# Kernel optimization log

Measured on AMD Instinct MI355X. Metric: run time of the kernel, lower is better.

Reference implementation:

```python
import jax, jax.numpy as jnp
import numpy as np
from jax import lax

BATCH, CH, SEQ, D_MODEL = 4, 8, 1024, 512
D_STATE, D_CONV, EXPAND = 16, 4, 2
D_INNER = EXPAND * D_MODEL
DT_RANK = (D_MODEL + 15) // 16  # math.ceil(d_model / 16) as in mamba_ssm


def _silu(v):
    return v * jax.nn.sigmoid(v)


def setup_inputs() -> dict:
    key = jax.random.key(0)
    ks = jax.random.split(key, 8)
    s = lambda fan: 1.0 / np.sqrt(fan)
    x = jax.random.normal(ks[0], (BATCH, CH, SEQ, D_MODEL), jnp.float32)
    W_in = jax.random.normal(ks[1], (2 * D_INNER, D_MODEL), jnp.float32) * s(D_MODEL)
    conv_w = jax.random.normal(ks[2], (D_INNER, D_CONV), jnp.float32) * s(D_CONV)
    conv_b = jnp.zeros((D_INNER,), jnp.float32)
    W_xproj = jax.random.normal(ks[3], (DT_RANK + 2 * D_STATE, D_INNER), jnp.float32) * s(D_INNER)
    W_dt = jax.random.normal(ks[4], (D_INNER, DT_RANK), jnp.float32) * s(DT_RANK)
    # dt bias ~ inverse-softplus of dt in [1e-3, 0.1] (mamba init)
    dt0 = jnp.exp(jax.random.uniform(ks[5], (D_INNER,), jnp.float32) * (np.log(0.1) - np.log(1e-3)) + np.log(1e-3))
    b_dt = dt0 + jnp.log(-jnp.expm1(-dt0))
    A_log = jnp.log(jnp.broadcast_to(jnp.arange(1, D_STATE + 1, dtype=jnp.float32), (D_INNER, D_STATE)))
    D = jnp.ones((D_INNER,), jnp.float32)
    W_out = jax.random.normal(ks[6], (D_MODEL, D_INNER), jnp.float32) * s(D_INNER)
    return {"x": x, "W_in": W_in, "conv_w": conv_w, "conv_b": conv_b,
            "W_xproj": W_xproj, "W_dt": W_dt, "b_dt": b_dt,
            "A_log": A_log, "D": D, "W_out": W_out}


def _mamba(u, W_in, conv_w, conv_b, W_xproj, W_dt, b_dt, A_log, D, W_out):
    # u: (B, L, d_model)
    Bn, L, _ = u.shape
    xz = u @ W_in.T                                  # (B, L, 2*d_inner)
    xs, z = jnp.split(xz, 2, axis=-1)
    # depthwise causal conv1d, padding=d_conv-1, truncated to L
    xt = jnp.pad(xs.transpose(0, 2, 1), ((0, 0), (0, 0), (D_CONV - 1, 0)))  # (B, d_inner, L+pad)
    xc = lax.conv_general_dilated(xt, conv_w[:, None, :], (1,), 'VALID',
                                  feature_group_count=D_INNER,
                                  dimension_numbers=('NCH', 'OIH', 'NCH'))   # (B, d_inner, L)
    xs = _silu((xc + conv_b[None, :, None]).transpose(0, 2, 1))              # (B, L, d_inner)
    x_dbl = xs @ W_xproj.T                           # (B, L, dt_rank + 2*d_state)
    dt_in = x_dbl[..., :DT_RANK]
    Bm = x_dbl[..., DT_RANK:DT_RANK + D_STATE]       # (B, L, d_state)
    Cm = x_dbl[..., DT_RANK + D_STATE:]              # (B, L, d_state)
    dt = jax.nn.softplus(dt_in @ W_dt.T + b_dt)      # (B, L, d_inner)
    A = -jnp.exp(A_log)                              # (d_inner, d_state)

    def step(h, inp):
        dt_t, B_t, C_t, x_t = inp                    # (B,di), (B,ds), (B,ds), (B,di)
        dA = jnp.exp(dt_t[..., None] * A)            # (B, di, ds)
        h = dA * h + (dt_t * x_t)[..., None] * B_t[:, None, :]
        y = jnp.einsum('bds,bs->bd', h, C_t)
        return h, y

    h0 = jnp.zeros((Bn, D_INNER, D_STATE), xs.dtype)
    xsL = (dt.transpose(1, 0, 2), Bm.transpose(1, 0, 2), Cm.transpose(1, 0, 2), xs.transpose(1, 0, 2))
    _, ys = lax.scan(step, h0, xsL)                  # ys: (L, B, d_inner)
    y = ys.transpose(1, 0, 2) + xs * D
    y = y * _silu(z)
    return y @ W_out.T                               # (B, L, d_model)


def reference(x, W_in, conv_w, conv_b, W_xproj, W_dt, b_dt, A_log, D, W_out):
    b, c, L, dm = x.shape
    # shared Mamba weights over channels -> fold channel into batch (== per-channel loop)
    u = x.reshape(b * c, L, dm)
    out = _mamba(u, W_in, conv_w, conv_b, W_xproj, W_dt, b_dt, A_log, D, W_out)
    return out.reshape(b, c, L, dm)
```

## Files before the change

kernel.cpp:

```cpp
#include <hip/hip_runtime.h>
#include <hip/hip_bf16.h>
#include <math.h>

#define BATCHN   4
#define CHN      8
#define SEQ      1024
#define DMODEL   512
#define DSTATE   16
#define DCONV    4
#define DINNER   1024
#define DTRANK   32
#define NROWS    32768
#define XD       64
#define NBC      32

#define GCH   16
#define CLEN  (SEQ / GCH)
#define SUB   32
#define PSLOT 17

#define CSPL  8
#define CTS   (SEQ / CSPL)

enum { EPI_NONE = 0, EPI_GATE = 1, EPI_GATE_PACK = 2 };

__device__ __forceinline__ float siluf(float v) {
    return v / (1.0f + expf(-v));
}
__device__ __forceinline__ float softplus_fast(float v) {
    return (v > 20.0f) ? v : __logf(1.0f + __expf(v));
}

typedef short short8 __attribute__((ext_vector_type(8)));
typedef float floatx4 __attribute__((ext_vector_type(4)));

__device__ __forceinline__ unsigned short f2bf_rne(float f) {
    unsigned int u = __float_as_uint(f);
    u += 0x7fffu + ((u >> 16) & 1u);
    return (unsigned short)(u >> 16);
}
__device__ __forceinline__ float bf2f(unsigned short h) {
    return __uint_as_float(((unsigned int)h) << 16);
}

__device__ __forceinline__ unsigned short* lds_pt(unsigned short (*arr)[32],
                                                  int row, int slot) {
    return &arr[row][(slot ^ ((row >> 1) & 3)) << 3];
}
__device__ __forceinline__ const unsigned short* lds_pt(
        const unsigned short (*arr)[32], int row, int slot) {
    return &arr[row][(slot ^ ((row >> 1) & 3)) << 3];
}

__global__ __launch_bounds__(256)
void split_w(const float* __restrict__ W, unsigned char* __restrict__ W2,
             int R, int K) {
    const int KB = K >> 5;
    const int idx = blockIdx.x * 256 + threadIdx.x;
    if (idx >= R * KB) return;
    const int row = idx / KB;
    const int kb  = idx - row * KB;
    const float* src = W + (size_t)row * K + kb * 32;
    unsigned short h[32], l[32];
#pragma unroll
    for (int e = 0; e < 32; e += 4) {
        const float4 v = *(const float4*)(src + e);
        const float vv[4] = {v.x, v.y, v.z, v.w};
#pragma unroll
        for (int q = 0; q < 4; ++q) {
            const unsigned short hi = f2bf_rne(vv[q]);
            h[e + q] = hi;
            l[e + q] = f2bf_rne(vv[q] - bf2f(hi));
        }
    }
    unsigned char* dst = W2 + ((size_t)row * KB + kb) * 128;
    union { short8 v; unsigned short u[8]; } pk;
#pragma unroll
    for (int c = 0; c < 4; ++c) {
#pragma unroll
        for (int e = 0; e < 8; ++e) pk.u[e] = h[c * 8 + e];
        *(short8*)(dst + c * 16) = pk.v;
    }
#pragma unroll
    for (int c = 0; c < 4; ++c) {
#pragma unroll
        for (int e = 0; e < 8; ++e) pk.u[e] = l[c * 8 + e];
        *(short8*)(dst + 64 + c * 16) = pk.v;
    }
}

template <bool A_PRE, bool B_PRE, int EPI>
__global__ __launch_bounds__(256, 2)
void gemm_split(const float* __restrict__ Af, const unsigned char* __restrict__ A2,
                int lda,
                const float* __restrict__ Bf, const unsigned char* __restrict__ B2,
                int ldb,
                float* __restrict__ C, int ldc,
                int K) {
    __shared__ __align__(16) unsigned short Ah[128][32];
    __shared__ __align__(16) unsigned short Al[128][32];
    __shared__ __align__(16) unsigned short Bh[128][32];
    __shared__ __align__(16) unsigned short Bl[128][32];

    const int tid  = threadIdx.x;
    const int lane = tid & 63;
    const int wv   = tid >> 6;
    const int quad = lane >> 4;
    const int m16  = lane & 15;
    const int wm   = (wv & 1) * 64;
    const int wn   = (wv >> 1) * 64;
    const int m0   = blockIdx.y * 128;
    const int n0   = blockIdx.x * 128;

    const int srow = tid >> 1;
    const int skb  = (tid & 1) * 16;
    const int ssl  = skb >> 3;

    const unsigned char* aptr = nullptr;
    const unsigned char* bptr = nullptr;
    if constexpr (A_PRE)
        aptr = A2 + (size_t)(m0 + srow) * (K >> 5) * 128 + 2 * skb;
    if constexpr (B_PRE)
        bptr = B2 + (size_t)(n0 + srow) * (K >> 5) * 128 + 2 * skb;

    floatx4 acc[4][4];
#pragma unroll
    for (int i = 0; i < 4; ++i)
#pragma unroll
        for (int j = 0; j < 4; ++j) acc[i][j] = (floatx4){0.f, 0.f, 0.f, 0.f};

    union U { short8 v; unsigned short u[8]; };

    for (int k0 = 0; k0 < K; k0 += 32) {
        short8 pa0, pa1, pa2, pa3;
        U ah0, ah1, al0, al1;
        if constexpr (A_PRE) {
            pa0 = *(const short8*)(aptr);
            pa1 = *(const short8*)(aptr + 16);
            pa2 = *(const short8*)(aptr + 64);
            pa3 = *(const short8*)(aptr + 80);
            aptr += 128;
        } else {
            const float* ap = Af + (size_t)(m0 + srow) * lda + k0 + skb;
            const float4 a0 = *(const float4*)(ap + 0);
            const float4 a1 = *(const float4*)(ap + 4);
            const float4 a2 = *(const float4*)(ap + 8);
            const float4 a3 = *(const float4*)(ap + 12);
            const float af[16] = {a0.x, a0.y, a0.z, a0.w, a1.x, a1.y, a1.z, a1.w,
                                  a2.x, a2.y, a2.z, a2.w, a3.x, a3.y, a3.z, a3.w};
#pragma unroll
            for (int e = 0; e < 8; ++e) {
                const unsigned short ha = f2bf_rne(af[e]);
                ah0.u[e] = ha; al0.u[e] = f2bf_rne(af[e] - bf2f(ha));
                const unsigned short hb = f2bf_rne(af[8 + e]);
                ah1.u[e] = hb; al1.u[e] = f2bf_rne(af[8 + e] - bf2f(hb));
            }
        }

        short8 pb0, pb1, pb2, pb3;
        U bh0, bh1, bl0, bl1;
        if constexpr (B_PRE) {
            pb0 = *(const short8*)(bptr);
            pb1 = *(const short8*)(bptr + 16);
            pb2 = *(const short8*)(bptr + 64);
            pb3 = *(const short8*)(bptr + 80);
            bptr += 128;
        } else {
            const float* bp = Bf + (size_t)(n0 + srow) * ldb + k0 + skb;
            const float4 b0 = *(const float4*)(bp + 0);
            const float4 b1 = *(const float4*)(bp + 4);
            const float4 b2 = *(const float4*)(bp + 8);
            const float4 b3 = *(const float4*)(bp + 12);
            const float bf[16] = {b0.x, b0.y, b0.z, b0.w, b1.x, b1.y, b1.z, b1.w,
                                  b2.x, b2.y, b2.z, b2.w, b3.x, b3.y, b3.z, b3.w};
#pragma unroll
            for (int e = 0; e < 8; ++e) {
                const unsigned short ha = f2bf_rne(bf[e]);
                bh0.u[e] = ha; bl0.u[e] = f2bf_rne(bf[e] - bf2f(ha));
                const unsigned short hb = f2bf_rne(bf[8 + e]);
                bh1.u[e] = hb; bl1.u[e] = f2bf_rne(bf[8 + e] - bf2f(hb));
            }
        }

        __syncthreads();
        if constexpr (A_PRE) {
            *(short8*)lds_pt(Ah, srow, ssl)     = pa0;
            *(short8*)lds_pt(Ah, srow, ssl | 1) = pa1;
            *(short8*)lds_pt(Al, srow, ssl)     = pa2;
            *(short8*)lds_pt(Al, srow, ssl | 1) = pa3;
        } else {
            *(short8*)lds_pt(Ah, srow, ssl)     = ah0.v;
            *(short8*)lds_pt(Ah, srow, ssl | 1) = ah1.v;
            *(short8*)lds_pt(Al, srow, ssl)     = al0.v;
            *(short8*)lds_pt(Al, srow, ssl | 1) = al1.v;
        }
        if constexpr (B_PRE) {
            *(short8*)lds_pt(Bh, srow, ssl)     = pb0;
            *(short8*)lds_pt(Bh, srow, ssl | 1) = pb1;
            *(short8*)lds_pt(Bl, srow, ssl)     = pb2;
            *(short8*)lds_pt(Bl, srow, ssl | 1) = pb3;
        } else {
            *(short8*)lds_pt(Bh, srow, ssl)     = bh0.v;
            *(short8*)lds_pt(Bh, srow, ssl | 1) = bh1.v;
            *(short8*)lds_pt(Bl, srow, ssl)     = bl0.v;
            *(short8*)lds_pt(Bl, srow, ssl | 1) = bl1.v;
        }
        __syncthreads();

        short8 a_h[4], a_l[4], b_h[4], b_l[4];
#pragma unroll
        for (int i = 0; i < 4; ++i) {
            a_h[i] = *(const short8*)lds_pt(Ah, wm + i * 16 + m16, quad);
            a_l[i] = *(const short8*)lds_pt(Al, wm + i * 16 + m16, quad);
            b_h[i] = *(const short8*)lds_pt(Bh, wn + i * 16 + m16, quad);
            b_l[i] = *(const short8*)lds_pt(Bl, wn + i * 16 + m16, quad);
        }
#pragma unroll
        for (int i = 0; i < 4; ++i)
#pragma unroll
            for (int j = 0; j < 4; ++j) {
                acc[i][j] = __builtin_amdgcn_mfma_f32_16x16x32_bf16(
                    a_h[i], b_h[j], acc[i][j], 0, 0, 0);
                acc[i][j] = __builtin_amdgcn_mfma_f32_16x16x32_bf16(
                    a_l[i], b_h[j], acc[i][j], 0, 0, 0);
                acc[i][j] = __builtin_amdgcn_mfma_f32_16x16x32_bf16(
                    a_h[i], b_l[j], acc[i][j], 0, 0, 0);
            }
    }

    if constexpr (EPI != EPI_GATE_PACK) {
#pragma unroll
        for (int i = 0; i < 4; ++i)
#pragma unroll
            for (int j = 0; j < 4; ++j) {
                const int col = n0 + wn + j * 16 + m16;
#pragma unroll
                for (int r = 0; r < 4; ++r) {
                    const int row = m0 + wm + i * 16 + quad * 4 + r;
                    const size_t off = (size_t)row * ldc + col;
                    const float v = acc[i][j][r];
                    if (EPI == EPI_NONE) C[off] = v;
                    else                 C[off] = C[off] * siluf(v);
                }
            }
    } else {
        unsigned char* Y2 = (unsigned char*)C;
        const size_t rowbytes = (size_t)ldc * 4;
#pragma unroll
        for (int i = 0; i < 4; ++i) {
            const int rbase = m0 + wm + i * 16 + quad * 4;
            float cold[4][4];
#pragma unroll
            for (int j = 0; j < 4; ++j) {
                const int col = n0 + wn + j * 16 + m16;
#pragma unroll
                for (int r = 0; r < 4; ++r)
                    cold[j][r] = C[(size_t)(rbase + r) * ldc + col];
            }
            asm volatile("s_waitcnt vmcnt(0)" ::: "memory");
#pragma unroll
            for (int j = 0; j < 4; ++j) {
                const int col = n0 + wn + j * 16 + m16;
                const int kb  = col >> 5;
                const unsigned off = (unsigned)(col & 31) * 2;
#pragma unroll
                for (int r = 0; r < 4; ++r) {
                    const int row = rbase + r;
                    const float g = cold[j][r] * siluf(acc[i][j][r]);
                    const unsigned short hi = f2bf_rne(g);
                    const unsigned short lo = f2bf_rne(g - bf2f(hi));
                    unsigned char* bp = Y2 + (size_t)row * rowbytes + (size_t)kb * 128;
                    *(unsigned short*)(bp + off)      = hi;
                    *(unsigned short*)(bp + 64 + off) = lo;
                }
            }
        }
    }
}

#define TBM 64
#define TBN 64
#define TBK 16

__global__ __launch_bounds__(256)
void gemm_atb(const float* __restrict__ A, int lda,
              const float* __restrict__ B, int ldb,
              float* __restrict__ C, int ldc,
              int K) {
    __shared__ float As[TBM][TBK + 1];
    __shared__ float Bs[TBN][TBK + 1];

    const int tid = threadIdx.x;
    const int tx = tid & 15;
    const int ty = tid >> 4;
    const int m0 = blockIdx.y * TBM;
    const int n0 = blockIdx.x * TBN;

    const int lr = tid >> 2;
    const int lc = (tid & 3) * 4;

    float acc[4][4];
#pragma unroll
    for (int i = 0; i < 4; ++i)
#pragma unroll
        for (int j = 0; j < 4; ++j) acc[i][j] = 0.0f;

    for (int k0 = 0; k0 < K; k0 += TBK) {
        const float4 av = *(const float4*)(A + (size_t)(m0 + lr) * lda + k0 + lc);
        const float4 bv = *(const float4*)(B + (size_t)(n0 + lr) * ldb + k0 + lc);
        As[lr][lc + 0] = av.x; As[lr][lc + 1] = av.y;
        As[lr][lc + 2] = av.z; As[lr][lc + 3] = av.w;
        Bs[lr][lc + 0] = bv.x; Bs[lr][lc + 1] = bv.y;
        Bs[lr][lc + 2] = bv.z; Bs[lr][lc + 3] = bv.w;
        __syncthreads();

#pragma unroll
        for (int kk = 0; kk < TBK; ++kk) {
            float a[4], b[4];
#pragma unroll
            for (int i = 0; i < 4; ++i) a[i] = As[ty * 4 + i][kk];
#pragma unroll
            for (int j = 0; j < 4; ++j) b[j] = Bs[tx * 4 + j][kk];
#pragma unroll
            for (int i = 0; i < 4; ++i)
#pragma unroll
                for (int j = 0; j < 4; ++j) acc[i][j] += a[i] * b[j];
        }
        __syncthreads();
    }

#pragma unroll
    for (int i = 0; i < 4; ++i) {
        const int r = m0 + ty * 4 + i;
#pragma unroll
        for (int j = 0; j < 4; ++j) {
            const int c = n0 + tx * 4 + j;
            C[(size_t)r * ldc + c] = acc[i][j];
        }
    }
}

__global__ __launch_bounds__(256)
void halo_save(const float* __restrict__ xs, float* __restrict__ halo) {
    const int idx = blockIdx.x * 256 + threadIdx.x;
    if (idx >= NBC * (CSPL - 1) * 3 * DINNER) return;
    const int d  = idx & (DINNER - 1);
    int r = idx >> 10;
    const int j  = r % 3;  r /= 3;
    const int sp = (r % (CSPL - 1)) + 1;
    const int b  = r / (CSPL - 1);
    halo[(((size_t)b * CSPL + sp) * 3 + j) * DINNER + d] =
        xs[((size_t)b * SEQ + sp * CTS - 3 + j) * DINNER + d];
}

__global__ __launch_bounds__(256)
void conv_split_silu(float* __restrict__ xs,
                     const float* __restrict__ conv_w,
                     const float* __restrict__ conv_b,
                     const float* __restrict__ halo) {
    const int gid = blockIdx.x * 256 + threadIdx.x;
    const int d  = gid & (DINNER - 1);
    const int sp = (gid >> 10) & (CSPL - 1);
    const int b  = gid >> 13;
    const float w0 = conv_w[d * DCONV + 0];
    const float w1 = conv_w[d * DCONV + 1];
    const float w2 = conv_w[d * DCONV + 2];
    const float w3 = conv_w[d * DCONV + 3];
    const float cb = conv_b[d];
    float x0, x1, x2;
    if (sp == 0) {
        x0 = 0.0f; x1 = 0.0f; x2 = 0.0f;
    } else {
        const float* hsrc = halo + (((size_t)b * CSPL + sp) * 3) * DINNER + d;
        x0 = hsrc[0];
        x1 = hsrc[DINNER];
        x2 = hsrc[2 * DINNER];
    }
    size_t p = ((size_t)b * SEQ + sp * CTS) * DINNER + d;
    for (int t = 0; t < CTS; ++t, p += DINNER) {
        const float xv = xs[p];
        const float acc = cb + w0 * x0 + w1 * x1 + w2 * x2 + w3 * xv;
        xs[p] = siluf(acc);
        x0 = x1; x1 = x2; x2 = xv;
    }
}

__device__ __forceinline__ size_t ps_idx(int c, int b, int slot, int d) {
    return ((size_t)(c * NBC + b) * PSLOT + slot) * DINNER + d;
}

template <int PASS>
__global__ __launch_bounds__(256)
void scan_chunk_kernel(float* __restrict__ xs,
                       const float* __restrict__ x_dbl,
                       const float* __restrict__ W_dt,
                       const float* __restrict__ b_dt,
                       const float* __restrict__ A_log,
                       const float* __restrict__ Dp,
                       float* __restrict__ ps) {
    const int tid = threadIdx.x;
    const int c  = blockIdx.x & (GCH - 1);
    const int dg = (blockIdx.x >> 4) & 3;
    const int b  = blockIdx.x >> 6;
    const int d  = (dg << 8) + tid;

    if (PASS == 0 && c == GCH - 1) return;

    float wdt[DTRANK];
#pragma unroll
    for (int k = 0; k < DTRANK; ++k) wdt[k] = W_dt[d * DTRANK + k];
    const float bdt = b_dt[d];
    const float Dv = Dp[d];

    float a[DSTATE], h[DSTATE];
    bool afast = true;
#pragma unroll
    for (int s = 0; s < DSTATE; ++s) {
        a[s] = -expf(A_log[d * DSTATE + s]);
        afast = afast && (fabsf(a[s] + (float)(s + 1)) <= 3e-3f * (float)(s + 1));
    }

    float dtsum = 0.0f;
#pragma unroll
    for (int s = 0; s < DSTATE; ++s) h[s] = 0.0f;

    if (PASS == 1) {
        for (int j = 0; j < c; ++j) {
            const float dsj = ps[ps_idx(j, b, 0, d)];
            if (afast) {
                const float F = __expf(dsj * a[0]);
                float P = F;
#pragma unroll
                for (int s = 0; s < DSTATE; ++s) {
                    h[s] = fmaf(P, h[s], ps[ps_idx(j, b, 1 + s, d)]);
                    P *= F;
                }
            } else {
#pragma unroll
                for (int s = 0; s < DSTATE; ++s)
                    h[s] = fmaf(__expf(dsj * a[s]), h[s],
                                ps[ps_idx(j, b, 1 + s, d)]);
            }
        }
    }

    __shared__ float bc[SUB][XD];
    const size_t brow = (size_t)b * SEQ + (size_t)c * CLEN;

    for (int t0 = 0; t0 < CLEN; t0 += SUB) {
        __syncthreads();
        if (PASS == 0) {
            for (int e = tid; e < SUB * 12; e += 256) {
                const int tt = e / 12;
                const int c4 = (e - tt * 12) * 4;
                const float4 v = *(const float4*)(x_dbl + (brow + t0 + tt) * XD + c4);
                bc[tt][c4 + 0] = v.x; bc[tt][c4 + 1] = v.y;
                bc[tt][c4 + 2] = v.z; bc[tt][c4 + 3] = v.w;
            }
        } else {
            for (int e = tid; e < SUB * 16; e += 256) {
                const int tt = e >> 4;
                const int c4 = (e & 15) * 4;
                const float4 v = *(const float4*)(x_dbl + (brow + t0 + tt) * XD + c4);
                bc[tt][c4 + 0] = v.x; bc[tt][c4 + 1] = v.y;
                bc[tt][c4 + 2] = v.z; bc[tt][c4 + 3] = v.w;
            }
        }
        __syncthreads();

        for (int tt = 0; tt < SUB; ++tt) {
            float g0 = 0.0f, g1 = 0.0f, g2 = 0.0f, g3 = 0.0f;
#pragma unroll
            for (int k = 0; k < DTRANK; k += 4) {
                const float4 q = *(const float4*)&bc[tt][k];
                g0 = fmaf(q.x, wdt[k + 0], g0);
                g1 = fmaf(q.y, wdt[k + 1], g1);
                g2 = fmaf(q.z, wdt[k + 2], g2);
                g3 = fmaf(q.w, wdt[k + 3], g3);
            }
            const float dtv = softplus_fast(bdt + ((g0 + g1) + (g2 + g3)));
            if (PASS == 0) dtsum += dtv;

            union F4 { float4 v; float f[4]; };
            F4 Bv[4], Cv[4];
#pragma unroll
            for (int q = 0; q < 4; ++q)
                Bv[q].v = *(const float4*)&bc[tt][DTRANK + q * 4];
            if (PASS == 1) {
#pragma unroll
                for (int q = 0; q < 4; ++q)
                    Cv[q].v = *(const float4*)&bc[tt][DTRANK + DSTATE + q * 4];
            }

            const size_t row = brow + t0 + tt;
            const float xv = xs[row * DINNER + d];
            const float pre = dtv * xv;
            float y0 = 0.0f, y1 = 0.0f;
            if (afast) {
                const float E = __expf(dtv * a[0]);
                float dA = E;
#pragma unroll
                for (int s = 0; s < DSTATE; ++s) {
                    h[s] = fmaf(dA, h[s], pre * Bv[s >> 2].f[s & 3]);
                    if (PASS == 1) {
                        if (s & 1) y1 = fmaf(h[s], Cv[s >> 2].f[s & 3], y1);
                        else       y0 = fmaf(h[s], Cv[s >> 2].f[s & 3], y0);
                    }
                    dA *= E;
                }
            } else {
#pragma unroll
                for (int s = 0; s < DSTATE; ++s) {
                    const float dA = __expf(dtv * a[s]);
                    h[s] = fmaf(dA, h[s], pre * Bv[s >> 2].f[s & 3]);
                    if (PASS == 1) {
                        if (s & 1) y1 = fmaf(h[s], Cv[s >> 2].f[s & 3], y1);
                        else       y0 = fmaf(h[s], Cv[s >> 2].f[s & 3], y0);
                    }
                }
            }
            if (PASS == 1) xs[row * DINNER + d] = fmaf(xv, Dv, y0 + y1);
        }
    }

    if (PASS == 0) {
        ps[ps_idx(c, b, 0, d)] = dtsum;
#pragma unroll
        for (int s = 0; s < DSTATE; ++s)
            ps[ps_idx(c, b, 1 + s, d)] = h[s];
    }
}

extern "C" void kernel_launch(void* const* d_in, const int* in_sizes, int n_in,
                              void* d_out, int out_size, void* d_ws, size_t ws_size,
                              hipStream_t stream) {
    const float* x       = (const float*)d_in[0];
    const float* W_in    = (const float*)d_in[1];
    const float* conv_w  = (const float*)d_in[2];
    const float* conv_b  = (const float*)d_in[3];
    const float* W_xproj = (const float*)d_in[4];
    const float* W_dt    = (const float*)d_in[5];
    const float* b_dt    = (const float*)d_in[6];
    const float* A_log   = (const float*)d_in[7];
    const float* Dp      = (const float*)d_in[8];
    const float* W_out   = (const float*)d_in[9];
    float* out = (float*)d_out;

    float* xs    = (float*)d_ws;
    float* x_dbl = out;
    float* ps    = out + (size_t)NROWS * XD;
    unsigned char* w2in = (unsigned char*)(out + 11534336);
    float* halo  = out + 12582912;

    const size_t xs_bytes = (size_t)NROWS * DINNER * 4;
    unsigned char* w2out = (unsigned char*)d_ws + xs_bytes;
    const bool have_wout = ws_size >= xs_bytes + (size_t)DMODEL * (DINNER / 32) * 128;

    dim3 blk(256);

    split_w<<<(2048 * 16) / 256, blk, 0, stream>>>(W_in, w2in, 2048, DMODEL);
    if (have_wout)
        split_w<<<(512 * 32) / 256, blk, 0, stream>>>(W_out, w2out, DMODEL, DINNER);

    gemm_split<false, true, EPI_NONE><<<dim3(DINNER / 128, NROWS / 128), blk, 0, stream>>>(
        x, nullptr, DMODEL, nullptr, w2in, 0, xs, DINNER, DMODEL);

    halo_save<<<(NBC * (CSPL - 1) * 3 * DINNER) / 256, blk, 0, stream>>>(xs, halo);
    conv_split_silu<<<NBC * CSPL * DINNER / 256, blk, 0, stream>>>(
        xs, conv_w, conv_b, halo);

    gemm_atb<<<dim3(XD / TBN, NROWS / TBM), blk, 0, stream>>>(
        xs, DINNER, W_xproj, DINNER, x_dbl, XD, DINNER);

    scan_chunk_kernel<0><<<NBC * 4 * GCH, blk, 0, stream>>>(
        xs, x_dbl, W_dt, b_dt, A_log, Dp, ps);
    scan_chunk_kernel<1><<<NBC * 4 * GCH, blk, 0, stream>>>(
        xs, x_dbl, W_dt, b_dt, A_log, Dp, ps);

    gemm_split<false, true, EPI_GATE_PACK><<<dim3(DINNER / 128, NROWS / 128), blk, 0, stream>>>(
        x, nullptr, DMODEL, nullptr, w2in + (size_t)1024 * 16 * 128, 0, xs, DINNER, DMODEL);

    if (have_wout)
        gemm_split<true, true, EPI_NONE><<<dim3(DMODEL / 128, NROWS / 128), blk, 0, stream>>>(
            nullptr, (const unsigned char*)xs, 0, nullptr, w2out, 0, out, DMODEL, DINNER);
    else
        gemm_split<true, false, EPI_NONE><<<dim3(DMODEL / 128, NROWS / 128), blk, 0, stream>>>(
            nullptr, (const unsigned char*)xs, 0, W_out, nullptr, DINNER, out, DMODEL, DINNER);
}
```

Measured before the change: 924.6 us.

## Use split-bf16 MFMA for x_proj GEMM, pre-split x, batch scan x loads

```diff
diff --git a/kernel.cpp b/kernel.cpp
--- a/kernel.cpp
+++ b/kernel.cpp
@@ -278,66 +278,114 @@
     }
 }
 
-#define TBM 64
-#define TBN 64
-#define TBK 16
-
-__global__ __launch_bounds__(256)
-void gemm_atb(const float* __restrict__ A, int lda,
-              const float* __restrict__ B, int ldb,
-              float* __restrict__ C, int ldc,
-              int K) {
-    __shared__ float As[TBM][TBK + 1];
-    __shared__ float Bs[TBN][TBK + 1];
-
-    const int tid = threadIdx.x;
-    const int tx = tid & 15;
-    const int ty = tid >> 4;
-    const int m0 = blockIdx.y * TBM;
-    const int n0 = blockIdx.x * TBN;
-
-    const int lr = tid >> 2;
-    const int lc = (tid & 3) * 4;
-
-    float acc[4][4];
+__global__ __launch_bounds__(256, 2)
+void gemm_xproj(const float* __restrict__ A, int lda,
+                const unsigned char* __restrict__ B2,
+                float* __restrict__ C, int ldc,
+                int K) {
+    __shared__ __align__(16) unsigned short Ah[128][32];
+    __shared__ __align__(16) unsigned short Al[128][32];
+    __shared__ __align__(16) unsigned short Bh[64][32];
+    __shared__ __align__(16) unsigned short Bl[64][32];
+
+    const int tid  = threadIdx.x;
+    const int lane = tid & 63;
+    const int wv   = tid >> 6;
+    const int quad = lane >> 4;
+    const int m16  = lane & 15;
+    const int wm   = (wv & 1) * 64;
+    const int wn   = (wv >> 1) * 32;
+    const int m0   = blockIdx.x * 128;
+
+    const int srow = tid >> 1;
+    const int skb  = (tid & 1) * 16;
+    const int ssl  = skb >> 3;
+
+    const unsigned char* bptr = B2 + (size_t)srow * (K >> 5) * 128 + 2 * skb;
+    const bool bstage = tid < 128;
+
+    floatx4 acc[4][2];
 #pragma unroll
     for (int i = 0; i < 4; ++i)
 #pragma unroll
-        for (int j = 0; j < 4; ++j) acc[i][j] = 0.0f;
-
-    for (int k0 = 0; k0 < K; k0 += TBK) {
-        const float4 av = *(const float4*)(A + (size_t)(m0 + lr) * lda + k0 + lc);
-        const float4 bv = *(const float4*)(B + (size_t)(n0 + lr) * ldb + k0 + lc);
-        As[lr][lc + 0] = av.x; As[lr][lc + 1] = av.y;
-        As[lr][lc + 2] = av.z; As[lr][lc + 3] = av.w;
-        Bs[lr][lc + 0] = bv.x; Bs[lr][lc + 1] = bv.y;
-        Bs[lr][lc + 2] = bv.z; Bs[lr][lc + 3] = bv.w;
+        for (int j = 0; j < 2; ++j) acc[i][j] = (floatx4){0.f, 0.f, 0.f, 0.f};
+
+    union U { short8 v; unsigned short u[8]; };
+
+    for (int k0 = 0; k0 < K; k0 += 32) {
+        const float* ap = A + (size_t)(m0 + srow) * lda + k0 + skb;
+        const float4 a0 = *(const float4*)(ap + 0);
+        const float4 a1 = *(const float4*)(ap + 4);
+        const float4 a2 = *(const float4*)(ap + 8);
+        const float4 a3 = *(const float4*)(ap + 12);
+        const float af[16] = {a0.x, a0.y, a0.z, a0.w, a1.x, a1.y, a1.z, a1.w,
+                              a2.x, a2.y, a2.z, a2.w, a3.x, a3.y, a3.z, a3.w};
+        short8 pb0, pb1, pb2, pb3;
+        if (bstage) {
+            pb0 = *(const short8*)(bptr);
+            pb1 = *(const short8*)(bptr + 16);
+            pb2 = *(const short8*)(bptr + 64);
+            pb3 = *(const short8*)(bptr + 80);
+        }
+        bptr += 128;
+
+        U ah0, ah1, al0, al1;
+#pragma unroll
+        for (int e = 0; e < 8; ++e) {
+            const unsigned short ha = f2bf_rne(af[e]);
+            ah0.u[e] = ha; al0.u[e] = f2bf_rne(af[e] - bf2f(ha));
+            const unsigned short hb = f2bf_rne(af[8 + e]);
+            ah1.u[e] = hb; al1.u[e] = f2bf_rne(af[8 + e] - bf2f(hb));
+        }
+
         __syncthreads();
-
-#pragma unroll
-        for (int kk = 0; kk < TBK; ++kk) {
-            float a[4], b[4];
-#pragma unroll
-            for (int i = 0; i < 4; ++i) a[i] = As[ty * 4 + i][kk];
-#pragma unroll
-            for (int j = 0; j < 4; ++j) b[j] = Bs[tx * 4 + j][kk];
-#pragma unroll
-            for (int i = 0; i < 4; ++i)
-#pragma unroll
-                for (int j = 0; j < 4; ++j) acc[i][j] += a[i] * b[j];
+        *(short8*)lds_pt(Ah, srow, ssl)     = ah0.v;
+        *(short8*)lds_pt(Ah, srow, ssl | 1) = ah1.v;
+        *(short8*)lds_pt(Al, srow, ssl)     = al0.v;
+        *(short8*)lds_pt(Al, srow, ssl | 1) = al1.v;
+        if (bstage) {
+            *(short8*)lds_pt(Bh, srow, ssl)     = pb0;
+            *(short8*)lds_pt(Bh, srow, ssl | 1) = pb1;
+            *(short8*)lds_pt(Bl, srow, ssl)     = pb2;
+            *(short8*)lds_pt(Bl, srow, ssl | 1) = pb3;
         }
         __syncthreads();
-    }
-
-#pragma unroll
-    for (int i = 0; i < 4; ++i) {
-        const int r = m0 + ty * 4 + i;
-#pragma unroll
-        for (int j = 0; j < 4; ++j) {
-            const int c = n0 + tx * 4 + j;
-            C[(size_t)r * ldc + c] = acc[i][j];
-        }
-    }
+
+        short8 a_h[4], a_l[4], b_h[2], b_l[2];
+#pragma unroll
+        for (int i = 0; i < 4; ++i) {
+            a_h[i] = *(const short8*)lds_pt(Ah, wm + i * 16 + m16, quad);
+            a_l[i] = *(const short8*)lds_pt(Al, wm + i * 16 + m16, quad);
+        }
+#pragma unroll
+        for (int j = 0; j < 2; ++j) {
+            b_h[j] = *(const short8*)lds_pt(Bh, wn + j * 16 + m16, quad);
+            b_l[j] = *(const short8*)lds_pt(Bl, wn + j * 16 + m16, quad);
+        }
+#pragma unroll
+        for (int i = 0; i < 4; ++i)
+#pragma unroll
+            for (int j = 0; j < 2; ++j) {
+                acc[i][j] = __builtin_amdgcn_mfma_f32_16x16x32_bf16(
+                    a_h[i], b_h[j], acc[i][j], 0, 0, 0);
+                acc[i][j] = __builtin_amdgcn_mfma_f32_16x16x32_bf16(
+                    a_l[i], b_h[j], acc[i][j], 0, 0, 0);
+                acc[i][j] = __builtin_amdgcn_mfma_f32_16x16x32_bf16(
+                    a_h[i], b_l[j], acc[i][j], 0, 0, 0);
+            }
+    }
+
+#pragma unroll
+    for (int i = 0; i < 4; ++i)
+#pragma unroll
+        for (int j = 0; j < 2; ++j) {
+            const int col = wn + j * 16 + m16;
+#pragma unroll
+            for (int r = 0; r < 4; ++r) {
+                const int row = m0 + wm + i * 16 + quad * 4 + r;
+                C[(size_t)row * ldc + col] = acc[i][j][r];
+            }
+        }
 }
 
 __global__ __launch_bounds__(256)
@@ -468,58 +516,69 @@
         }
         __syncthreads();
 
-        for (int tt = 0; tt < SUB; ++tt) {
-            float g0 = 0.0f, g1 = 0.0f, g2 = 0.0f, g3 = 0.0f;
-#pragma unroll
-            for (int k = 0; k < DTRANK; k += 4) {
-                const float4 q = *(const float4*)&bc[tt][k];
-                g0 = fmaf(q.x, wdt[k + 0], g0);
-                g1 = fmaf(q.y, wdt[k + 1], g1);
-                g2 = fmaf(q.z, wdt[k + 2], g2);
-                g3 = fmaf(q.w, wdt[k + 3], g3);
-            }
-            const float dtv = softplus_fast(bdt + ((g0 + g1) + (g2 + g3)));
-            if (PASS == 0) dtsum += dtv;
-
-            union F4 { float4 v; float f[4]; };
-            F4 Bv[4], Cv[4];
-#pragma unroll
-            for (int q = 0; q < 4; ++q)
-                Bv[q].v = *(const float4*)&bc[tt][DTRANK + q * 4];
-            if (PASS == 1) {
+        for (int gg = 0; gg < SUB / 8; ++gg) {
+            float xr[8];
+            {
+                const float* xp = xs + (brow + t0 + gg * 8) * DINNER + d;
+#pragma unroll
+                for (int e = 0; e < 8; ++e) xr[e] = xp[(size_t)e * DINNER];
+            }
+            float* xw = xs + (brow + t0 + gg * 8) * DINNER + d;
+
+#pragma unroll
+            for (int t8 = 0; t8 < 8; ++t8) {
+                const int tt = gg * 8 + t8;
+                float g0 = 0.0f, g1 = 0.0f, g2 = 0.0f, g3 = 0.0f;
+#pragma unroll
+                for (int k = 0; k < DTRANK; k += 4) {
+                    const float4 q = *(const float4*)&bc[tt][k];
+                    g0 = fmaf(q.x, wdt[k + 0], g0);
+                    g1 = fmaf(q.y, wdt[k + 1], g1);
+                    g2 = fmaf(q.z, wdt[k + 2], g2);
+                    g3 = fmaf(q.w, wdt[k + 3], g3);
+                }
+                const float dtv = softplus_fast(bdt + ((g0 + g1) + (g2 + g3)));
+                if (PASS == 0) dtsum += dtv;
+
+                union F4 { float4 v; float f[4]; };
+                F4 Bv[4], Cv[4];
 #pragma unroll
                 for (int q = 0; q < 4; ++q)
-                    Cv[q].v = *(const float4*)&bc[tt][DTRANK + DSTATE + q * 4];
-            }
-
-            const size_t row = brow + t0 + tt;
-            const float xv = xs[row * DINNER + d];
-            const float pre = dtv * xv;
-            float y0 = 0.0f, y1 = 0.0f;
-            if (afast) {
-                const float E = __expf(dtv * a[0]);
-                float dA = E;
-#pragma unroll
-                for (int s = 0; s < DSTATE; ++s) {
-                    h[s] = fmaf(dA, h[s], pre * Bv[s >> 2].f[s & 3]);
-                    if (PASS == 1) {
-                        if (s & 1) y1 = fmaf(h[s], Cv[s >> 2].f[s & 3], y1);
-                        else       y0 = fmaf(h[s], Cv[s >> 2].f[s & 3], y0);
+                    Bv[q].v = *(const float4*)&bc[tt][DTRANK + q * 4];
+                if (PASS == 1) {
+#pragma unroll
+                    for (int q = 0; q < 4; ++q)
+                        Cv[q].v = *(const float4*)&bc[tt][DTRANK + DSTATE + q * 4];
+                }
+
+                const float xv = xr[t8];
+                const float pre = dtv * xv;
+                float y0 = 0.0f, y1 = 0.0f;
+                if (afast) {
+                    const float E = __expf(dtv * a[0]);
+                    float dA = E;
+#pragma unroll
+                    for (int s = 0; s < DSTATE; ++s) {
+                        h[s] = fmaf(dA, h[s], pre * Bv[s >> 2].f[s & 3]);
+                        if (PASS == 1) {
+                            if (s & 1) y1 = fmaf(h[s], Cv[s >> 2].f[s & 3], y1);
+                            else       y0 = fmaf(h[s], Cv[s >> 2].f[s & 3], y0);
+                        }
+                        dA *= E;
                     }
-                    dA *= E;
-                }
-            } else {
-#pragma unroll
-                for (int s = 0; s < DSTATE; ++s) {
-                    const float dA = __expf(dtv * a[s]);
-                    h[s] = fmaf(dA, h[s], pre * Bv[s >> 2].f[s & 3]);
-                    if (PASS == 1) {
-                        if (s & 1) y1 = fmaf(h[s], Cv[s >> 2].f[s & 3], y1);
-                        else       y0 = fmaf(h[s], Cv[s >> 2].f[s & 3], y0);
+                } else {
+#pragma unroll
+                    for (int s = 0; s < DSTATE; ++s) {
+                        const float dA = __expf(dtv * a[s]);
+                        h[s] = fmaf(dA, h[s], pre * Bv[s >> 2].f[s & 3]);
+                        if (PASS == 1) {
+                            if (s & 1) y1 = fmaf(h[s], Cv[s >> 2].f[s & 3], y1);
+                            else       y0 = fmaf(h[s], Cv[s >> 2].f[s & 3], y0);
+                        }
                     }
                 }
-            }
-            if (PASS == 1) xs[row * DINNER + d] = fmaf(xv, Dv, y0 + y1);
+                if (PASS == 1) xw[(size_t)t8 * DINNER] = fmaf(xv, Dv, y0 + y1);
+            }
         }
     }
 
@@ -551,34 +610,49 @@
     float* ps    = out + (size_t)NROWS * XD;
     unsigned char* w2in = (unsigned char*)(out + 11534336);
     float* halo  = out + 12582912;
-
-    const size_t xs_bytes = (size_t)NROWS * DINNER * 4;
+    unsigned char* wxp2 = (unsigned char*)(out + 13631488);
+
+    const size_t xs_bytes   = (size_t)NROWS * DINNER * 4;
+    const size_t wout_bytes = (size_t)DMODEL * (DINNER / 32) * 128;
+    const size_t x2_bytes   = (size_t)NROWS * (DMODEL / 32) * 128;
     unsigned char* w2out = (unsigned char*)d_ws + xs_bytes;
-    const bool have_wout = ws_size >= xs_bytes + (size_t)DMODEL * (DINNER / 32) * 128;
+    unsigned char* x2    = (unsigned char*)d_ws + xs_bytes + wout_bytes;
+    const bool have_wout = ws_size >= xs_bytes + wout_bytes;
+    const bool have_x2   = ws_size >= xs_bytes + wout_bytes + x2_bytes;
 
     dim3 blk(256);
 
     split_w<<<(2048 * 16) / 256, blk, 0, stream>>>(W_in, w2in, 2048, DMODEL);
+    split_w<<<(64 * 32 + 255) / 256, blk, 0, stream>>>(W_xproj, wxp2, XD, DINNER);
     if (have_wout)
         split_w<<<(512 * 32) / 256, blk, 0, stream>>>(W_out, w2out, DMODEL, DINNER);
-
-    gemm_split<false, true, EPI_NONE><<<dim3(DINNER / 128, NROWS / 128), blk, 0, stream>>>(
-        x, nullptr, DMODEL, nullptr, w2in, 0, xs, DINNER, DMODEL);
+    if (have_x2)
+        split_w<<<(NROWS * 16) / 256, blk, 0, stream>>>(x, x2, NROWS, DMODEL);
+
+    if (have_x2)
+        gemm_split<true, true, EPI_NONE><<<dim3(DINNER / 128, NROWS / 128), blk, 0, stream>>>(
+            nullptr, x2, 0, nullptr, w2in, 0, xs, DINNER, DMODEL);
+    else
+        gemm_split<false, true, EPI_NONE><<<dim3(DINNER / 128, NROWS / 128), blk, 0, stream>>>(
+            x, nullptr, DMODEL, nullptr, w2in, 0, xs, DINNER, DMODEL);
 
     halo_save<<<(NBC * (CSPL - 1) * 3 * DINNER) / 256, blk, 0, stream>>>(xs, halo);
     conv_split_silu<<<NBC * CSPL * DINNER / 256, blk, 0, stream>>>(
         xs, conv_w, conv_b, halo);
 
-    gemm_atb<<<dim3(XD / TBN, NROWS / TBM), blk, 0, stream>>>(
-        xs, DINNER, W_xproj, DINNER, x_dbl, XD, DINNER);
+    gemm_xproj<<<NROWS / 128, blk, 0, stream>>>(xs, DINNER, wxp2, x_dbl, XD, DINNER);
 
     scan_chunk_kernel<0><<<NBC * 4 * GCH, blk, 0, stream>>>(
         xs, x_dbl, W_dt, b_dt, A_log, Dp, ps);
     scan_chunk_kernel<1><<<NBC * 4 * GCH, blk, 0, stream>>>(
         xs, x_dbl, W_dt, b_dt, A_log, Dp, ps);
 
-    gemm_split<false, true, EPI_GATE_PACK><<<dim3(DINNER / 128, NROWS / 128), blk, 0, stream>>>(
-        x, nullptr, DMODEL, nullptr, w2in + (size_t)1024 * 16 * 128, 0, xs, DINNER, DMODEL);
+    if (have_x2)
+        gemm_split<true, true, EPI_GATE_PACK><<<dim3(DINNER / 128, NROWS / 128), blk, 0, stream>>>(
+            nullptr, x2, 0, nullptr, w2in + (size_t)1024 * 16 * 128, 0, xs, DINNER, DMODEL);
+    else
+        gemm_split<false, true, EPI_GATE_PACK><<<dim3(DINNER / 128, NROWS / 128), blk, 0, stream>>>(
+            x, nullptr, DMODEL, nullptr, w2in + (size_t)1024 * 16 * 128, 0, xs, DINNER, DMODEL);
 
     if (have_wout)
         gemm_split<true, true, EPI_NONE><<<dim3(DMODEL / 128, NROWS / 128), blk, 0, stream>>>(
```

Result: faster. 901.6 us (-2.5%).
